# Performance work log

Measured on AMD Instinct MI355X. Metric: run time of the kernel, lower is better.

## Reference

```python
import jax, jax.numpy as jnp
import numpy as np

ROUTING_ITERS = 3
EPS = 1e-8

def _squash_elem(s):
    # Faithful to torch squash with dim=-1 over a trailing size-1 axis: elementwise.
    sq = s * s
    return (sq / (1.0 + sq)) * s / jnp.sqrt(sq + EPS)

def setup_inputs() -> dict:
    key = jax.random.key(0)
    k1, k2 = jax.random.split(key)
    x = jax.random.normal(k1, (64, 1152, 64), dtype=jnp.float32)            # [B, N_routes, in_ch]
    route_weights = jax.random.normal(k2, (32, 1152, 64, 64), dtype=jnp.float32)  # [C, N, out, in]
    return {"x": x, "route_weights": route_weights}

def reference(x, route_weights):
    B = x.shape[0]
    C, N, O, _ = route_weights.shape
    # u_hat: [B, C, N, O]  (torch trailing size-1 dim dropped; squash/sums over it are elementwise)
    u_hat = jnp.einsum('cnoi,bni->bcno', route_weights, x)
    b_ij = jnp.zeros((B, C, N, 1), dtype=x.dtype)
    v_j = None
    for i in range(ROUTING_ITERS):
        c_ij = jax.nn.softmax(b_ij, axis=1)                  # over capsules
        s_j = jnp.sum(c_ij * u_hat, axis=2, keepdims=True)   # [B, C, 1, O]
        v_j = _squash_elem(s_j)
        if i < ROUTING_ITERS - 1:
            # torch: b_ij + (u_hat * v_j).sum(-1, keepdim) over size-1 dim -> broadcasts to [B,C,N,O]
            b_ij = b_ij + u_hat * v_j
    return v_j[:, :, 0, :]  # [B, C, O]
```

## Files before the change

### kernel.cpp

```cpp
#include <hip/hip_runtime.h>
#include <hip/hip_bf16.h>

typedef short short8v __attribute__((ext_vector_type(8)));
typedef float float4v __attribute__((ext_vector_type(4)));

constexpr int Bb = 64;
constexpr int Cc = 32;
constexpr int Nn = 1152;
constexpr int Oo = 64;
constexpr int Ii = 64;
constexpr int NCH = 32;
constexpr int CHN = 36;
constexpr int OT  = 16;

__device__ __forceinline__ unsigned short bf16_rne(float f) {
    unsigned u = __float_as_uint(f);
    u += 0x7FFFu + ((u >> 16) & 1u);
    return (unsigned short)(u >> 16);
}
__device__ __forceinline__ float bf16_f(unsigned short h) {
    return __uint_as_float(((unsigned)h) << 16);
}
__device__ __forceinline__ float squash_elem(float s) {
    float sq = s * s;
    return (sq / (1.f + sq)) * s / sqrtf(sq + 1e-8f);
}

__device__ __forceinline__ void barrier_nodrain() {
    asm volatile("s_waitcnt lgkmcnt(0)" ::: "memory");
    __builtin_amdgcn_s_barrier();
    asm volatile("" ::: "memory");
}

__device__ __forceinline__ void split8(const float4& f0, const float4& f1,
                                       short8v& h, short8v& lo) {
    float a[8] = {f0.x, f0.y, f0.z, f0.w, f1.x, f1.y, f1.z, f1.w};
#pragma unroll
    for (int e = 0; e < 8; ++e) {
        unsigned short hb = bf16_rne(a[e]);
        h[e] = (short)hb;
        lo[e] = (short)bf16_rne(a[e] - bf16_f(hb));
    }
}

__global__ __launch_bounds__(256) void prep_xt(const float* __restrict__ x,
                                               unsigned short* __restrict__ xh,
                                               unsigned short* __restrict__ xl) {
    const int n = blockIdx.x, t = threadIdx.x;
    const int b = t >> 2, q = t & 3;
    const float* src = x + ((size_t)b * Nn + n) * Ii + q * 16;
    float4 v0 = *(const float4*)(src);
    float4 v1 = *(const float4*)(src + 4);
    float4 v2 = *(const float4*)(src + 8);
    float4 v3 = *(const float4*)(src + 12);
    short8v h0, l0, h1, l1;
    split8(v0, v1, h0, l0);
    split8(v2, v3, h1, l1);
    size_t dst = (size_t)n * (Bb * Ii) + b * Ii + q * 16;
    *(short8v*)(xh + dst) = h0;
    *(short8v*)(xh + dst + 8) = h1;
    *(short8v*)(xl + dst) = l0;
    *(short8v*)(xl + dst + 8) = l1;
}

template <int MODE>
__global__ __launch_bounds__(256, 2) void caps_pass(
    const float* __restrict__ w, const unsigned short* __restrict__ xh,
    const unsigned short* __restrict__ xl, const float* __restrict__ V,
    float* __restrict__ part) {
    __shared__ unsigned short sh[2][128 * 64];
    __shared__ unsigned short sl[2][128 * 64];

    const int t = threadIdx.x;
    const int l = t & 63, wv = t >> 6;
    const int ch = blockIdx.x, ot = blockIdx.y;
    const int obase = ot * 4;
    const int kg = l >> 4;
    const int lm = l & 15;
    const int n0 = ch * CHN;
    const int sw = (lm & 7) << 3;

    float Vreg[8][4];
    if constexpr (MODE == 1) {
#pragma unroll
        for (int t8 = 0; t8 < 8; ++t8)
#pragma unroll
            for (int r = 0; r < 4; ++r) {
                int b = 16 * wv + 4 * kg + r;
                int c = 4 * t8 + ((l >> 2) & 3);
                int o = obase + (l & 3);
                Vreg[t8][r] = V[((size_t)b * Cc + c) * Oo + o];
            }
    }
    float4v acc4[8];
    float accs[8][4];
#pragma unroll
    for (int t8 = 0; t8 < 8; ++t8) {
        acc4[t8] = (float4v){0.f, 0.f, 0.f, 0.f};
#pragma unroll
        for (int r = 0; r < 4; ++r) accs[t8][r] = 0.f;
    }

    const int i0 = (t & 15) * 4;
    const int colb = t >> 4;
    float4 L0[8], L1[8];

    auto issue = [&](int n, float4(&ld)[8]) {
#pragma unroll
        for (int k = 0; k < 8; ++k) {
            int col = colb + 16 * k;
            int c = col >> 2, olc = col & 3;
            ld[k] = *(const float4*)(
                w + (((size_t)c * Nn + n) * Oo + obase + olc) * Ii + i0);
        }
    };
    auto writebuf = [&](unsigned short* dh, unsigned short* dl,
                        const float4(&ld)[8]) {
#pragma unroll
        for (int k = 0; k < 8; ++k) {
            int col = colb + 16 * k;
            int off = col * 64 + (i0 ^ ((col & 7) << 3));
            float a[4] = {ld[k].x, ld[k].y, ld[k].z, ld[k].w};
            ushort4 H, L;
            unsigned short* hp = (unsigned short*)&H;
            unsigned short* lp = (unsigned short*)&L;
#pragma unroll
            for (int e = 0; e < 4; ++e) {
                unsigned short hb = bf16_rne(a[e]);
                hp[e] = hb;
                lp[e] = bf16_rne(a[e] - bf16_f(hb));
            }
            *(ushort4*)(dh + off) = H;
            *(ushort4*)(dl + off) = L;
        }
    };

    struct AFrag { short8v h0, l0, h1, l1; };
    auto loadA = [&](int n) {
        AFrag A;
        const size_t xoff =
            (size_t)n * (Bb * Ii) + (16 * wv + lm) * Ii + kg * 8;
        A.h0 = *(const short8v*)(xh + xoff);
        A.l0 = *(const short8v*)(xl + xoff);
        A.h1 = *(const short8v*)(xh + xoff + 32);
        A.l1 = *(const short8v*)(xl + xoff + 32);
        return A;
    };

    auto compute = [&](const unsigned short* bh_, const unsigned short* bl_,
                       const AFrag& A) {
        float u[8][4];
#pragma unroll
        for (int t8 = 0; t8 < 8; ++t8) {
            int row = 16 * t8 + lm;
            int c0 = row * 64 + ((kg * 8) ^ sw);
            int c1 = row * 64 + (((kg * 8) + 32) ^ sw);
            short8v bh0 = *(const short8v*)(bh_ + c0);
            short8v bl0 = *(const short8v*)(bl_ + c0);
            short8v bh1 = *(const short8v*)(bh_ + c1);
            short8v bl1 = *(const short8v*)(bl_ + c1);
            float4v a;
            if constexpr (MODE == 0) a = acc4[t8];
            else a = (float4v){0.f, 0.f, 0.f, 0.f};
            a = __builtin_amdgcn_mfma_f32_16x16x32_bf16(A.h0, bh0, a, 0, 0, 0);
            a = __builtin_amdgcn_mfma_f32_16x16x32_bf16(A.l0, bh0, a, 0, 0, 0);
            a = __builtin_amdgcn_mfma_f32_16x16x32_bf16(A.h0, bl0, a, 0, 0, 0);
            a = __builtin_amdgcn_mfma_f32_16x16x32_bf16(A.h1, bh1, a, 0, 0, 0);
            a = __builtin_amdgcn_mfma_f32_16x16x32_bf16(A.l1, bh1, a, 0, 0, 0);
            a = __builtin_amdgcn_mfma_f32_16x16x32_bf16(A.h1, bl1, a, 0, 0, 0);
            if constexpr (MODE == 0) {
                acc4[t8] = a;
            } else {
                u[t8][0] = a[0]; u[t8][1] = a[1];
                u[t8][2] = a[2]; u[t8][3] = a[3];
            }
        }
        if constexpr (MODE == 1) {
#pragma unroll
            for (int r = 0; r < 4; ++r) {
                float m = -1e30f;
#pragma unroll
                for (int t8 = 0; t8 < 8; ++t8)
                    m = fmaxf(m, u[t8][r] * Vreg[t8][r]);
                m = fmaxf(m, __shfl_xor(m, 4));
                m = fmaxf(m, __shfl_xor(m, 8));
                float Z = 0.f;
#pragma unroll
                for (int t8 = 0; t8 < 8; ++t8) {
                    float e = __expf(u[t8][r] * Vreg[t8][r] - m);
                    Z += e;
                    u[t8][r] *= e;
                }
                Z += __shfl_xor(Z, 4);
                Z += __shfl_xor(Z, 8);
                float rz = 1.f / Z;
#pragma unroll
                for (int t8 = 0; t8 < 8; ++t8) accs[t8][r] += u[t8][r] * rz;
            }
        }
    };

    issue(n0, L0);
    writebuf(sh[0], sl[0], L0);
    issue(n0 + 1, L1);
    barrier_nodrain();

    for (int j = 0; j < CHN; j += 2) {
        AFrag A0 = loadA(n0 + j);
        if (j + 2 < CHN) issue(n0 + j + 2, L0);
        writebuf(sh[1], sl[1], L1);
        compute(sh[0], sl[0], A0);
        barrier_nodrain();
        AFrag A1 = loadA(n0 + j + 1);
        if (j + 3 < CHN) issue(n0 + j + 3, L1);
        if (j + 2 < CHN) writebuf(sh[0], sl[0], L0);
        compute(sh[1], sl[1], A1);
        barrier_nodrain();
    }

#pragma unroll
    for (int t8 = 0; t8 < 8; ++t8)
#pragma unroll
        for (int r = 0; r < 4; ++r) {
            int b = 16 * wv + 4 * kg + r;
            int c = 4 * t8 + ((l >> 2) & 3);
            int o = obase + (l & 3);
            float val = (MODE == 0) ? acc4[t8][r] : accs[t8][r];
            part[(((size_t)ch * Bb + b) * Cc + c) * Oo + o] = val;
        }
}

__global__ void reduce_caps(const float* __restrict__ part,
                            float* __restrict__ V, float* __restrict__ out,
                            int mode) {
    int bc = blockIdx.x;
    int o = threadIdx.x;
    size_t base = (size_t)bc * 64 + o;
    float s = 0.f;
    for (int c = 0; c < NCH; ++c) s += part[(size_t)c * (Bb * Cc * Oo) + base];
    if (mode == 0)      V[base] = squash_elem(s * (1.f / 32.f));
    else if (mode == 1) V[base] += squash_elem(s);
    else                out[base] = squash_elem(s);
}

extern "C" void kernel_launch(void* const* d_in, const int* in_sizes, int n_in,
                              void* d_out, int out_size, void* d_ws, size_t ws_size,
                              hipStream_t stream) {
    const float* x = (const float*)d_in[0];
    const float* w = (const float*)d_in[1];
    float* out = (float*)d_out;

    const size_t XE = (size_t)Bb * Nn * Ii;
    unsigned short* xh = (unsigned short*)d_ws;
    unsigned short* xl = xh + XE;
    float* part = (float*)(xl + XE);
    float* V = part + (size_t)NCH * Bb * Cc * Oo;

    prep_xt<<<Nn, 256, 0, stream>>>(x, xh, xl);

    caps_pass<0><<<dim3(NCH, OT), 256, 0, stream>>>(w, xh, xl, nullptr, part);
    reduce_caps<<<Bb * Cc, 64, 0, stream>>>(part, V, out, 0);
    caps_pass<1><<<dim3(NCH, OT), 256, 0, stream>>>(w, xh, xl, V, part);
    reduce_caps<<<Bb * Cc, 64, 0, stream>>>(part, V, out, 1);
    caps_pass<1><<<dim3(NCH, OT), 256, 0, stream>>>(w, xh, xl, V, part);
    reduce_caps<<<Bb * Cc, 64, 0, stream>>>(part, V, out, 2);
}
```

Measured before the change: 584.0 us.

## Retile capsule pass to 2x2 wave grid reusing B fragments across batch halves

```diff
diff --git a/kernel.cpp b/kernel.cpp
--- a/kernel.cpp
+++ b/kernel.cpp
@@ -73,33 +73,38 @@
 
     const int t = threadIdx.x;
     const int l = t & 63, wv = t >> 6;
+    const int wb = wv >> 1, wo = wv & 1;
     const int ch = blockIdx.x, ot = blockIdx.y;
     const int obase = ot * 4;
-    const int kg = l >> 4;
-    const int lm = l & 15;
+    const int kg = l >> 4, lm = l & 15;
     const int n0 = ch * CHN;
-    const int sw = (lm & 7) << 3;
-
-    float Vreg[8][4];
+    const int myc = lm >> 1;
+    const int myo = obase + 2 * wo + (lm & 1);
+
+    float Vreg[2][4][4];
     if constexpr (MODE == 1) {
 #pragma unroll
-        for (int t8 = 0; t8 < 8; ++t8)
-#pragma unroll
-            for (int r = 0; r < 4; ++r) {
-                int b = 16 * wv + 4 * kg + r;
-                int c = 4 * t8 + ((l >> 2) & 3);
-                int o = obase + (l & 3);
-                Vreg[t8][r] = V[((size_t)b * Cc + c) * Oo + o];
-            }
+        for (int bq = 0; bq < 2; ++bq)
+#pragma unroll
+            for (int t8 = 0; t8 < 4; ++t8)
+#pragma unroll
+                for (int r = 0; r < 4; ++r) {
+                    int b = 32 * wb + 16 * bq + 4 * kg + r;
+                    int c = 8 * t8 + myc;
+                    Vreg[bq][t8][r] =
+                        V[((size_t)b * Cc + c) * Oo + myo] * 1.44269504f;
+                }
     }
-    float4v acc4[8];
-    float accs[8][4];
-#pragma unroll
-    for (int t8 = 0; t8 < 8; ++t8) {
-        acc4[t8] = (float4v){0.f, 0.f, 0.f, 0.f};
-#pragma unroll
-        for (int r = 0; r < 4; ++r) accs[t8][r] = 0.f;
-    }
+    float4v acc4[2][4];
+    float accs[2][4][4];
+#pragma unroll
+    for (int bq = 0; bq < 2; ++bq)
+#pragma unroll
+        for (int t8 = 0; t8 < 4; ++t8) {
+            acc4[bq][t8] = (float4v){0.f, 0.f, 0.f, 0.f};
+#pragma unroll
+            for (int r = 0; r < 4; ++r) accs[bq][t8][r] = 0.f;
+        }
 
     const int i0 = (t & 15) * 4;
     const int colb = t >> 4;
@@ -109,9 +114,10 @@
 #pragma unroll
         for (int k = 0; k < 8; ++k) {
             int col = colb + 16 * k;
-            int c = col >> 2, olc = col & 3;
+            int c = (col & 63) >> 1;
+            int ol = 2 * (col >> 6) + (col & 1);
             ld[k] = *(const float4*)(
-                w + (((size_t)c * Nn + n) * Oo + obase + olc) * Ii + i0);
+                w + (((size_t)c * Nn + n) * Oo + obase + ol) * Ii + i0);
         }
     };
     auto writebuf = [&](unsigned short* dh, unsigned short* dl,
@@ -126,77 +132,89 @@
             unsigned short* lp = (unsigned short*)&L;
 #pragma unroll
             for (int e = 0; e < 4; ++e) {
-                unsigned short hb = bf16_rne(a[e]);
-                hp[e] = hb;
-                lp[e] = bf16_rne(a[e] - bf16_f(hb));
+                unsigned b = __float_as_uint(a[e]);
+                unsigned r = b + 0x7FFFu + ((b >> 16) & 1u);
+                hp[e] = (unsigned short)(r >> 16);
+                float res = a[e] - __uint_as_float(r & 0xFFFF0000u);
+                lp[e] = (unsigned short)(__float_as_uint(res) >> 16);
             }
             *(ushort4*)(dh + off) = H;
             *(ushort4*)(dl + off) = L;
         }
     };
 
-    struct AFrag { short8v h0, l0, h1, l1; };
-    auto loadA = [&](int n) {
-        AFrag A;
-        const size_t xoff =
-            (size_t)n * (Bb * Ii) + (16 * wv + lm) * Ii + kg * 8;
-        A.h0 = *(const short8v*)(xh + xoff);
-        A.l0 = *(const short8v*)(xl + xoff);
-        A.h1 = *(const short8v*)(xh + xoff + 32);
-        A.l1 = *(const short8v*)(xl + xoff + 32);
-        return A;
-    };
-
     auto compute = [&](const unsigned short* bh_, const unsigned short* bl_,
-                       const AFrag& A) {
-        float u[8][4];
-#pragma unroll
-        for (int t8 = 0; t8 < 8; ++t8) {
-            int row = 16 * t8 + lm;
-            int c0 = row * 64 + ((kg * 8) ^ sw);
-            int c1 = row * 64 + (((kg * 8) + 32) ^ sw);
-            short8v bh0 = *(const short8v*)(bh_ + c0);
-            short8v bl0 = *(const short8v*)(bl_ + c0);
-            short8v bh1 = *(const short8v*)(bh_ + c1);
-            short8v bl1 = *(const short8v*)(bl_ + c1);
-            float4v a;
-            if constexpr (MODE == 0) a = acc4[t8];
-            else a = (float4v){0.f, 0.f, 0.f, 0.f};
-            a = __builtin_amdgcn_mfma_f32_16x16x32_bf16(A.h0, bh0, a, 0, 0, 0);
-            a = __builtin_amdgcn_mfma_f32_16x16x32_bf16(A.l0, bh0, a, 0, 0, 0);
-            a = __builtin_amdgcn_mfma_f32_16x16x32_bf16(A.h0, bl0, a, 0, 0, 0);
-            a = __builtin_amdgcn_mfma_f32_16x16x32_bf16(A.h1, bh1, a, 0, 0, 0);
-            a = __builtin_amdgcn_mfma_f32_16x16x32_bf16(A.l1, bh1, a, 0, 0, 0);
-            a = __builtin_amdgcn_mfma_f32_16x16x32_bf16(A.h1, bl1, a, 0, 0, 0);
-            if constexpr (MODE == 0) {
-                acc4[t8] = a;
-            } else {
-                u[t8][0] = a[0]; u[t8][1] = a[1];
-                u[t8][2] = a[2]; u[t8][3] = a[3];
+                       int n) {
+        short8v Ah0[2], Al0[2], Ah1[2], Al1[2];
+#pragma unroll
+        for (int bq = 0; bq < 2; ++bq) {
+            const size_t xoff =
+                (size_t)n * (Bb * Ii) + (32 * wb + 16 * bq + lm) * Ii + kg * 8;
+            Ah0[bq] = *(const short8v*)(xh + xoff);
+            Al0[bq] = *(const short8v*)(xl + xoff);
+            Ah1[bq] = *(const short8v*)(xh + xoff + 32);
+            Al1[bq] = *(const short8v*)(xl + xoff + 32);
+        }
+
+        float u[2][4][4];
+#pragma unroll
+        for (int t8 = 0; t8 < 4; ++t8) {
+            int colL = 64 * wo + 16 * t8 + lm;
+            int base = colL * 64;
+            int key = (colL & 7) << 3;
+            int off0 = base + ((kg * 8) ^ key);
+            int off1 = base + ((kg * 8 + 32) ^ key);
+            short8v bh0 = *(const short8v*)(bh_ + off0);
+            short8v bl0 = *(const short8v*)(bl_ + off0);
+            short8v bh1 = *(const short8v*)(bh_ + off1);
+            short8v bl1 = *(const short8v*)(bl_ + off1);
+#pragma unroll
+            for (int bq = 0; bq < 2; ++bq) {
+                float4v a;
+                if constexpr (MODE == 0) a = acc4[bq][t8];
+                else a = (float4v){0.f, 0.f, 0.f, 0.f};
+                a = __builtin_amdgcn_mfma_f32_16x16x32_bf16(Ah0[bq], bh0, a, 0, 0, 0);
+                a = __builtin_amdgcn_mfma_f32_16x16x32_bf16(Al0[bq], bh0, a, 0, 0, 0);
+                a = __builtin_amdgcn_mfma_f32_16x16x32_bf16(Ah0[bq], bl0, a, 0, 0, 0);
+                a = __builtin_amdgcn_mfma_f32_16x16x32_bf16(Ah1[bq], bh1, a, 0, 0, 0);
+                a = __builtin_amdgcn_mfma_f32_16x16x32_bf16(Al1[bq], bh1, a, 0, 0, 0);
+                a = __builtin_amdgcn_mfma_f32_16x16x32_bf16(Ah1[bq], bl1, a, 0, 0, 0);
+                if constexpr (MODE == 0) {
+                    acc4[bq][t8] = a;
+                } else {
+                    u[bq][t8][0] = a[0]; u[bq][t8][1] = a[1];
+                    u[bq][t8][2] = a[2]; u[bq][t8][3] = a[3];
+                }
             }
         }
+
         if constexpr (MODE == 1) {
 #pragma unroll
-            for (int r = 0; r < 4; ++r) {
-                float m = -1e30f;
-#pragma unroll
-                for (int t8 = 0; t8 < 8; ++t8)
-                    m = fmaxf(m, u[t8][r] * Vreg[t8][r]);
-                m = fmaxf(m, __shfl_xor(m, 4));
-                m = fmaxf(m, __shfl_xor(m, 8));
-                float Z = 0.f;
-#pragma unroll
-                for (int t8 = 0; t8 < 8; ++t8) {
-                    float e = __expf(u[t8][r] * Vreg[t8][r] - m);
-                    Z += e;
-                    u[t8][r] *= e;
+            for (int bq = 0; bq < 2; ++bq)
+#pragma unroll
+                for (int r = 0; r < 4; ++r) {
+                    float l0 = u[bq][0][r] * Vreg[bq][0][r];
+                    float l1 = u[bq][1][r] * Vreg[bq][1][r];
+                    float l2 = u[bq][2][r] * Vreg[bq][2][r];
+                    float l3 = u[bq][3][r] * Vreg[bq][3][r];
+                    float m = fmaxf(fmaxf(l0, l1), fmaxf(l2, l3));
+                    m = fmaxf(m, __shfl_xor(m, 2));
+                    m = fmaxf(m, __shfl_xor(m, 4));
+                    m = fmaxf(m, __shfl_xor(m, 8));
+                    float e0 = exp2f(l0 - m);
+                    float e1 = exp2f(l1 - m);
+                    float e2 = exp2f(l2 - m);
+                    float e3 = exp2f(l3 - m);
+                    float Z = (e0 + e1) + (e2 + e3);
+                    Z += __shfl_xor(Z, 2);
+                    Z += __shfl_xor(Z, 4);
+                    Z += __shfl_xor(Z, 8);
+                    float rz = 1.f / Z;
+                    accs[bq][0][r] = fmaf(e0 * rz, u[bq][0][r], accs[bq][0][r]);
+                    accs[bq][1][r] = fmaf(e1 * rz, u[bq][1][r], accs[bq][1][r]);
+                    accs[bq][2][r] = fmaf(e2 * rz, u[bq][2][r], accs[bq][2][r]);
+                    accs[bq][3][r] = fmaf(e3 * rz, u[bq][3][r], accs[bq][3][r]);
                 }
-                Z += __shfl_xor(Z, 4);
-                Z += __shfl_xor(Z, 8);
-                float rz = 1.f / Z;
-#pragma unroll
-                for (int t8 = 0; t8 < 8; ++t8) accs[t8][r] += u[t8][r] * rz;
-            }
         }
     };
 
@@ -206,28 +224,27 @@
     barrier_nodrain();
 
     for (int j = 0; j < CHN; j += 2) {
-        AFrag A0 = loadA(n0 + j);
+        writebuf(sh[1], sl[1], L1);
         if (j + 2 < CHN) issue(n0 + j + 2, L0);
-        writebuf(sh[1], sl[1], L1);
-        compute(sh[0], sl[0], A0);
+        compute(sh[0], sl[0], n0 + j);
         barrier_nodrain();
-        AFrag A1 = loadA(n0 + j + 1);
+        if (j + 2 < CHN) writebuf(sh[0], sl[0], L0);
         if (j + 3 < CHN) issue(n0 + j + 3, L1);
-        if (j + 2 < CHN) writebuf(sh[0], sl[0], L0);
-        compute(sh[1], sl[1], A1);
+        compute(sh[1], sl[1], n0 + j + 1);
         barrier_nodrain();
     }
 
 #pragma unroll
-    for (int t8 = 0; t8 < 8; ++t8)
-#pragma unroll
-        for (int r = 0; r < 4; ++r) {
-            int b = 16 * wv + 4 * kg + r;
-            int c = 4 * t8 + ((l >> 2) & 3);
-            int o = obase + (l & 3);
-            float val = (MODE == 0) ? acc4[t8][r] : accs[t8][r];
-            part[(((size_t)ch * Bb + b) * Cc + c) * Oo + o] = val;
-        }
+    for (int bq = 0; bq < 2; ++bq)
+#pragma unroll
+        for (int t8 = 0; t8 < 4; ++t8)
+#pragma unroll
+            for (int r = 0; r < 4; ++r) {
+                int b = 32 * wb + 16 * bq + 4 * kg + r;
+                int c = 8 * t8 + myc;
+                float val = (MODE == 0) ? acc4[bq][t8][r] : accs[bq][t8][r];
+                part[(((size_t)ch * Bb + b) * Cc + c) * Oo + myo] = val;
+            }
 }
 
 __global__ void reduce_caps(const float* __restrict__ part,
```

Result: slower. 626.3 us (+7.2%).
